# Performance work log

Measured on AMD Instinct MI355X. Metric: run time of the kernel, lower is better.

## Reference

```python
import jax, jax.numpy as jnp
import numpy as np

N_HEADS = 16


def setup_inputs() -> dict:
    key = jax.random.key(0)
    k1, k2, k3, k4, k5 = jax.random.split(key, 5)
    B, T, C = 2, 2048, 1024
    x = jax.random.normal(k1, (B, T, C), dtype=jnp.float32)
    rotary_cos_sin = jax.random.normal(k2, (T, C // N_HEADS), dtype=jnp.float32)  # unused by forward
    c = jax.random.normal(k3, (B, C), dtype=jnp.float32)  # unused by forward
    # Linear weights, torch convention: y = x @ W.T
    W_qkv = jax.random.normal(k4, (3 * C, C), dtype=jnp.float32) * (1.0 / np.sqrt(C))
    W_out = jax.random.normal(k5, (C, C), dtype=jnp.float32) * (1.0 / np.sqrt(C))
    return {"x": x, "rotary_cos_sin": rotary_cos_sin, "c": c, "W_qkv": W_qkv, "W_out": W_out}


def reference(x, rotary_cos_sin, c, W_qkv, W_out):
    B, T, C = x.shape
    H = N_HEADS
    D = C // H
    # qkv projection (no bias)
    qkv = jnp.einsum('btc,fc->btf', x, W_qkv)          # [B,T,3C]
    q, k, v = jnp.split(qkv, 3, axis=-1)
    q = q.reshape(B, T, H, D)
    k = k.reshape(B, T, H, D)
    v = v.reshape(B, T, H, D)
    # manual attention: full TxT score matrix, as in the original
    att = jnp.einsum('bthd,bshd->bhts', q, k) * (1.0 / jnp.sqrt(jnp.asarray(D, x.dtype)))
    att = jax.nn.softmax(att, axis=-1)
    # attn_dropout / resid_dropout are identity at inference
    y = jnp.einsum('bhts,bshd->bthd', att, v).reshape(B, T, C)
    return jnp.einsum('btc,oc->bto', y, W_out)
```

## Files before the change

### kernel.cpp

```cpp
#include <hip/hip_runtime.h>
#include <hip/hip_bf16.h>

typedef __bf16 bf16;
typedef __attribute__((ext_vector_type(8))) __bf16 bf16x8;
typedef __attribute__((ext_vector_type(4))) float f32x4;

#define MFMA16(A, B, C) __builtin_amdgcn_mfma_f32_16x16x32_bf16((A), (B), (C), 0, 0, 0)

__device__ __forceinline__ void gload_lds16(const void* g, void* l) {
    __builtin_amdgcn_global_load_lds(
        (const __attribute__((address_space(1))) void*)g,
        (__attribute__((address_space(3))) void*)l,
        16, 0, 0);
}

__global__ __launch_bounds__(256) void cast_f32_bf16(
    const float* __restrict__ in, bf16* __restrict__ out)
{
    const int i = (blockIdx.x * 256 + threadIdx.x) * 8;
    const float4 a = *(const float4*)(in + i);
    const float4 b = *(const float4*)(in + i + 4);
    bf16x8 o;
    o[0] = (bf16)a.x; o[1] = (bf16)a.y; o[2] = (bf16)a.z; o[3] = (bf16)a.w;
    o[4] = (bf16)b.x; o[5] = (bf16)b.y; o[6] = (bf16)b.z; o[7] = (bf16)b.w;
    *(bf16x8*)(out + i) = o;
}

template <typename OutT>
__global__ __launch_bounds__(256) void gemm_bt128(
    const bf16* __restrict__ A, const bf16* __restrict__ B, OutT* __restrict__ C,
    int M, int N, int K)
{
    constexpr int BK = 32;
    __shared__ __align__(16) bf16 sA[128 * BK];
    __shared__ __align__(16) bf16 sB[128 * BK];

    const int tid  = threadIdx.x;
    const int lane = tid & 63;
    const int wave = tid >> 6;
    const int wr   = wave >> 1;
    const int wc   = wave & 1;
    const int bm   = blockIdx.y * 128;
    const int bn   = blockIdx.x * 128;

    f32x4 acc[4][4] = {};

    const size_t ldb = (size_t)K * 2;
    const int srow = wave * 32 + (lane >> 2);
    const int scol = (lane & 3) * 16;
    const char* Ab = (const char*)A + (size_t)(bm + srow) * ldb + scol;
    const char* Bb = (const char*)B + (size_t)(bn + srow) * ldb + scol;
    char* ldsA = (char*)sA + wave * 2048;
    char* ldsB = (char*)sB + wave * 2048;

    const int arow = wr * 64 + (lane & 15);
    const int brow = wc * 64 + (lane & 15);
    const int koff = (lane >> 4) * 8;

    for (int k0 = 0; k0 < K; k0 += BK) {
        __syncthreads();
        const size_t kb = (size_t)k0 * 2;
        gload_lds16(Ab + kb,                ldsA);
        gload_lds16(Ab + kb + 16 * ldb,     ldsA + 1024);
        gload_lds16(Bb + kb,                ldsB);
        gload_lds16(Bb + kb + 16 * ldb,     ldsB + 1024);
        __syncthreads();

        bf16x8 af[4], bfr[4];
#pragma unroll
        for (int m = 0; m < 4; ++m)
            af[m] = *(const bf16x8*)&sA[(arow + m * 16) * BK + koff];
#pragma unroll
        for (int n = 0; n < 4; ++n)
            bfr[n] = *(const bf16x8*)&sB[(brow + n * 16) * BK + koff];
#pragma unroll
        for (int m = 0; m < 4; ++m)
#pragma unroll
            for (int n = 0; n < 4; ++n)
                acc[m][n] = MFMA16(af[m], bfr[n], acc[m][n]);
    }

    const int crow0 = bm + wr * 64 + (lane >> 4) * 4;
    const int ccol0 = bn + wc * 64 + (lane & 15);
#pragma unroll
    for (int m = 0; m < 4; ++m)
#pragma unroll
        for (int n = 0; n < 4; ++n)
#pragma unroll
            for (int j = 0; j < 4; ++j)
                C[(size_t)(crow0 + m * 16 + j) * N + ccol0 + n * 16] = (OutT)acc[m][n][j];
}

__global__ __launch_bounds__(256) void attn64(
    const bf16* __restrict__ qkv, bf16* __restrict__ y)
{
    constexpr int T = 2048, Cd = 1024, F = 3072, D = 64, KV = 64;
    __shared__ __align__(16) bf16 sK[KV * D];
    __shared__ __align__(16) bf16 sVT[D * 72];
    __shared__ __align__(16) bf16 sP[4 * 16 * 72];

    const int tid  = threadIdx.x;
    const int lane = tid & 63;
    const int wave = tid >> 6;
    const int bh = blockIdx.y;
    const int b  = bh >> 4, h = bh & 15;
    const int q0 = blockIdx.x * 64;

    const bf16* qkvb = qkv + (size_t)b * T * F;
    const int qcol = h * D;
    const int kcol = Cd + h * D;
    const int vcol = 2 * Cd + h * D;

    const int qrow = q0 + wave * 16 + (lane & 15);
    bf16x8 qf[2];
#pragma unroll
    for (int kk = 0; kk < 2; ++kk)
        qf[kk] = *(const bf16x8*)(qkvb + (size_t)qrow * F + qcol + kk * 32 + (lane >> 4) * 8);

    f32x4 oacc[4] = {};
    float m_r[4] = {-1e30f, -1e30f, -1e30f, -1e30f};
    float l_r[4] = {};

    const int ksrow  = wave * 16 + (lane >> 3);
    const int kdbyte = 16 * ((lane & 7) ^ (lane >> 3));
    bf16* sPw = sP + wave * 16 * 72;

    for (int s0 = 0; s0 < T; s0 += KV) {
        __syncthreads();
        gload_lds16((const char*)qkvb + ((size_t)(s0 + ksrow) * F + kcol) * 2 + kdbyte,
                    (char*)sK + wave * 2048);
        gload_lds16((const char*)qkvb + ((size_t)(s0 + ksrow + 8) * F + kcol) * 2 + kdbyte,
                    (char*)sK + wave * 2048 + 1024);
#pragma unroll
        for (int r = 0; r < 2; ++r) {
            const int d0 = wave * 8 + r * 32;
            bf16x8 v = *(const bf16x8*)(qkvb + (size_t)(s0 + lane) * F + vcol + d0);
#pragma unroll
            for (int i = 0; i < 8; ++i) sVT[(d0 + i) * 72 + lane] = v[i];
        }
        __syncthreads();

        f32x4 sacc[4] = {};
#pragma unroll
        for (int kk = 0; kk < 2; ++kk) {
#pragma unroll
            for (int j = 0; j < 4; ++j) {
                const int krow = (lane & 15) + 16 * j;
                const int dlog = kk * 64 + (lane >> 4) * 16;
                bf16x8 kf = *(const bf16x8*)((const char*)sK + krow * 128 + (dlog ^ ((krow & 7) << 4)));
                sacc[j] = MFMA16(qf[kk], kf, sacc[j]);
            }
        }

#pragma unroll
        for (int r = 0; r < 4; ++r) {
            float mx = fmaxf(fmaxf(sacc[0][r], sacc[1][r]), fmaxf(sacc[2][r], sacc[3][r])) * 0.125f;
#pragma unroll
            for (int m = 1; m < 16; m <<= 1) mx = fmaxf(mx, __shfl_xor(mx, m));
            const float mn = fmaxf(m_r[r], mx);
            const float al = __expf(m_r[r] - mn);
            m_r[r] = mn;
            float rs = 0.f;
#pragma unroll
            for (int j = 0; j < 4; ++j) {
                const float p = __expf(sacc[j][r] * 0.125f - mn);
                rs += p;
                sPw[((lane >> 4) * 4 + r) * 72 + (lane & 15) + 16 * j] = (bf16)p;
            }
            l_r[r] = l_r[r] * al + rs;
#pragma unroll
            for (int n = 0; n < 4; ++n) oacc[n][r] *= al;
        }

#pragma unroll
        for (int kk = 0; kk < 2; ++kk) {
            bf16x8 pa = *(const bf16x8*)&sPw[(lane & 15) * 72 + kk * 32 + (lane >> 4) * 8];
#pragma unroll
            for (int n = 0; n < 4; ++n) {
                bf16x8 vf = *(const bf16x8*)&sVT[((lane & 15) + 16 * n) * 72 + kk * 32 + (lane >> 4) * 8];
                oacc[n] = MFMA16(pa, vf, oacc[n]);
            }
        }
    }

#pragma unroll
    for (int r = 0; r < 4; ++r) {
        float ls = l_r[r];
#pragma unroll
        for (int m = 1; m < 16; m <<= 1) ls += __shfl_xor(ls, m);
        const float inv = 1.f / ls;
        const int t = q0 + wave * 16 + (lane >> 4) * 4 + r;
#pragma unroll
        for (int n = 0; n < 4; ++n)
            y[(size_t)(b * T + t) * Cd + h * D + (lane & 15) + 16 * n] = (bf16)(oacc[n][r] * inv);
    }
}

extern "C" void kernel_launch(void* const* d_in, const int* in_sizes, int n_in,
                              void* d_out, int out_size, void* d_ws, size_t ws_size,
                              hipStream_t stream) {
    (void)in_sizes; (void)n_in; (void)out_size; (void)ws_size;
    const float* x    = (const float*)d_in[0];
    const float* Wqkv = (const float*)d_in[3];
    const float* Wout = (const float*)d_in[4];
    float* out = (float*)d_out;

    bf16* xb    = (bf16*)d_ws;
    bf16* wqkvb = xb    + (size_t)4096 * 1024;
    bf16* woutb = wqkvb + (size_t)3072 * 1024;
    bf16* qkv   = woutb + (size_t)1024 * 1024;
    bf16* yb    = qkv   + (size_t)4096 * 3072;

    cast_f32_bf16<<<4096 * 1024 / 2048, 256, 0, stream>>>(x, xb);
    cast_f32_bf16<<<3072 * 1024 / 2048, 256, 0, stream>>>(Wqkv, wqkvb);
    cast_f32_bf16<<<1024 * 1024 / 2048, 256, 0, stream>>>(Wout, woutb);

    gemm_bt128<bf16><<<dim3(3072 / 128, 4096 / 128), 256, 0, stream>>>(xb, wqkvb, qkv, 4096, 3072, 1024);
    attn64<<<dim3(2048 / 64, 2 * 16), 256, 0, stream>>>(qkv, yb);
    gemm_bt128<float><<<dim3(1024 / 128, 4096 / 128), 256, 0, stream>>>(yb, woutb, out, 4096, 1024, 1024);
}
```

Measured before the change: 253.1 us.

## Rewrite attention with 32x32 MFMA, transposed LDS reads and register-resident P

Replaces the 16x16 MFMA flash-attention kernel with one using 32x32x16 MFMA, 128 queries per block and 32 per wave. S is computed as K·Q^T so the probabilities stay in registers and are repacked via lane shuffles rather than written to LDS. V is loaded asynchronously into LDS and read with ds_read_b64_tr_b16 transposing loads instead of a manual scalar transpose. Softmax switches to exp2 with a folded scale. It adds intricate index swizzling and manual waitcnt scheduling, which raises correctness risk.

```diff
diff --git a/kernel.cpp b/kernel.cpp
--- a/kernel.cpp
+++ b/kernel.cpp
@@ -2,16 +2,33 @@
 #include <hip/hip_bf16.h>
 
 typedef __bf16 bf16;
+typedef __attribute__((ext_vector_type(4))) __bf16 bf16x4;
 typedef __attribute__((ext_vector_type(8))) __bf16 bf16x8;
 typedef __attribute__((ext_vector_type(4))) float f32x4;
+typedef __attribute__((ext_vector_type(16))) float f32x16;
 
 #define MFMA16(A, B, C) __builtin_amdgcn_mfma_f32_16x16x32_bf16((A), (B), (C), 0, 0, 0)
+#define MFMA32(A, B, C) __builtin_amdgcn_mfma_f32_32x32x16_bf16((A), (B), (C), 0, 0, 0)
+
+union U8 { unsigned w[4]; bf16x8 v; };
 
 __device__ __forceinline__ void gload_lds16(const void* g, void* l) {
     __builtin_amdgcn_global_load_lds(
         (const __attribute__((address_space(1))) void*)g,
         (__attribute__((address_space(3))) void*)l,
         16, 0, 0);
+}
+
+__device__ __forceinline__ unsigned pk2(float a, float b) {
+    union { bf16 h[2]; unsigned u; } t;
+    t.h[0] = (bf16)a; t.h[1] = (bf16)b;
+    return t.u;
+}
+
+__device__ __forceinline__ unsigned long long tr16(unsigned addr) {
+    unsigned long long r;
+    asm volatile("ds_read_b64_tr_b16 %0, %1" : "=v"(r) : "v"(addr));
+    return r;
 }
 
 __global__ __launch_bounds__(256) void cast_f32_bf16(
@@ -60,10 +77,10 @@
     for (int k0 = 0; k0 < K; k0 += BK) {
         __syncthreads();
         const size_t kb = (size_t)k0 * 2;
-        gload_lds16(Ab + kb,                ldsA);
-        gload_lds16(Ab + kb + 16 * ldb,     ldsA + 1024);
-        gload_lds16(Bb + kb,                ldsB);
-        gload_lds16(Bb + kb + 16 * ldb,     ldsB + 1024);
+        gload_lds16(Ab + kb,            ldsA);
+        gload_lds16(Ab + kb + 16 * ldb, ldsA + 1024);
+        gload_lds16(Bb + kb,            ldsB);
+        gload_lds16(Bb + kb + 16 * ldb, ldsB + 1024);
         __syncthreads();
 
         bf16x8 af[4], bfr[4];
@@ -91,109 +108,173 @@
                 C[(size_t)(crow0 + m * 16 + j) * N + ccol0 + n * 16] = (OutT)acc[m][n][j];
 }
 
-__global__ __launch_bounds__(256) void attn64(
+__global__ __launch_bounds__(256, 2) void attn32(
     const bf16* __restrict__ qkv, bf16* __restrict__ y)
 {
-    constexpr int T = 2048, Cd = 1024, F = 3072, D = 64, KV = 64;
-    __shared__ __align__(16) bf16 sK[KV * D];
-    __shared__ __align__(16) bf16 sVT[D * 72];
-    __shared__ __align__(16) bf16 sP[4 * 16 * 72];
-
-    const int tid  = threadIdx.x;
-    const int lane = tid & 63;
-    const int wave = tid >> 6;
-    const int bh = blockIdx.y;
-    const int b  = bh >> 4, h = bh & 15;
-    const int q0 = blockIdx.x * 64;
-
+    constexpr int T = 2048, F = 3072, Cd = 1024;
+    constexpr float c1 = 0.18033688011112042f;
+
+    __shared__ __align__(16) bf16 sK[64 * 64];
+    __shared__ __align__(16) bf16 sV[64 * 64];
+
+    const int tid = threadIdx.x, lane = tid & 63, wave = tid >> 6;
+    const int hi = lane >> 5, q5 = lane & 31;
+    const int bh = blockIdx.y, b = bh >> 4, h = bh & 15;
     const bf16* qkvb = qkv + (size_t)b * T * F;
-    const int qcol = h * D;
-    const int kcol = Cd + h * D;
-    const int vcol = 2 * Cd + h * D;
-
-    const int qrow = q0 + wave * 16 + (lane & 15);
-    bf16x8 qf[2];
-#pragma unroll
-    for (int kk = 0; kk < 2; ++kk)
-        qf[kk] = *(const bf16x8*)(qkvb + (size_t)qrow * F + qcol + kk * 32 + (lane >> 4) * 8);
-
-    f32x4 oacc[4] = {};
-    float m_r[4] = {-1e30f, -1e30f, -1e30f, -1e30f};
-    float l_r[4] = {};
-
-    const int ksrow  = wave * 16 + (lane >> 3);
-    const int kdbyte = 16 * ((lane & 7) ^ (lane >> 3));
-    bf16* sPw = sP + wave * 16 * 72;
-
-    for (int s0 = 0; s0 < T; s0 += KV) {
+    const int qcol = h * 64, kcol = Cd + h * 64, vcol = 2 * Cd + h * 64;
+
+    const int gq = blockIdx.x * 128 + wave * 32 + q5;
+    bf16x8 qf[4];
+#pragma unroll
+    for (int s = 0; s < 4; ++s)
+        qf[s] = *(const bf16x8*)(qkvb + (size_t)gq * F + qcol + s * 16 + hi * 8);
+
+    const int ck0 = (wave * 2 + 0) * 64 + lane, ck1 = ck0 + 64;
+    const int kvk0 = ck0 >> 3, d0k0 = ((ck0 & 7) ^ (kvk0 & 7)) << 3;
+    const int kvk1 = ck1 >> 3, d0k1 = ((ck1 & 7) ^ (kvk1 & 7)) << 3;
+    const int cv0 = ck0, cv1 = ck1;
+    const int kvv0 = ((cv0 >> 1) & 3) | (((cv0 >> 5) & 1) << 2) | (((cv0 >> 4) & 1) << 3) | (((cv0 >> 6) & 3) << 4);
+    const int dv0  = ((cv0 & 1) << 3) | (((cv0 >> 3) & 1) << 4) | (((cv0 >> 8) & 1) << 5);
+    const int kvv1 = ((cv1 >> 1) & 3) | (((cv1 >> 5) & 1) << 2) | (((cv1 >> 4) & 1) << 3) | (((cv1 >> 6) & 3) << 4);
+    const int dv1  = ((cv1 & 1) << 3) | (((cv1 >> 3) & 1) << 4) | (((cv1 >> 8) & 1) << 5);
+
+    const char* kq0 = (const char*)qkvb + (size_t)(kvk0 * F + kcol + d0k0) * 2;
+    const char* kq1 = (const char*)qkvb + (size_t)(kvk1 * F + kcol + d0k1) * 2;
+    const char* vq0 = (const char*)qkvb + (size_t)(kvv0 * F + vcol + dv0) * 2;
+    const char* vq1 = (const char*)qkvb + (size_t)(kvv1 * F + vcol + dv1) * 2;
+    char* dstK0 = (char*)sK + (wave * 2 + 0) * 1024;
+    char* dstK1 = (char*)sK + (wave * 2 + 1) * 1024;
+    char* dstV0 = (char*)sV + (wave * 2 + 0) * 1024;
+    char* dstV1 = (char*)sV + (wave * 2 + 1) * 1024;
+
+    const unsigned sVoff = (unsigned)(uintptr_t)(__attribute__((address_space(3))) char*)(void*)sV;
+    const unsigned trb = sVoff + 8u * (unsigned)lane;
+
+    const unsigned swz = (unsigned)(q5 & 7) << 4;
+
+    f32x16 oacc[2] = {};
+    float m_run = -3e38f, l_run = 0.f;
+
+    for (int s0 = 0; s0 < T; s0 += 64) {
         __syncthreads();
-        gload_lds16((const char*)qkvb + ((size_t)(s0 + ksrow) * F + kcol) * 2 + kdbyte,
-                    (char*)sK + wave * 2048);
-        gload_lds16((const char*)qkvb + ((size_t)(s0 + ksrow + 8) * F + kcol) * 2 + kdbyte,
-                    (char*)sK + wave * 2048 + 1024);
-#pragma unroll
-        for (int r = 0; r < 2; ++r) {
-            const int d0 = wave * 8 + r * 32;
-            bf16x8 v = *(const bf16x8*)(qkvb + (size_t)(s0 + lane) * F + vcol + d0);
-#pragma unroll
-            for (int i = 0; i < 8; ++i) sVT[(d0 + i) * 72 + lane] = v[i];
-        }
+        const size_t sb = (size_t)s0 * F * 2;
+        gload_lds16(kq0 + sb, dstK0);
+        gload_lds16(kq1 + sb, dstK1);
+        gload_lds16(vq0 + sb, dstV0);
+        gload_lds16(vq1 + sb, dstV1);
         __syncthreads();
 
-        f32x4 sacc[4] = {};
-#pragma unroll
-        for (int kk = 0; kk < 2; ++kk) {
-#pragma unroll
-            for (int j = 0; j < 4; ++j) {
-                const int krow = (lane & 15) + 16 * j;
-                const int dlog = kk * 64 + (lane >> 4) * 16;
-                bf16x8 kf = *(const bf16x8*)((const char*)sK + krow * 128 + (dlog ^ ((krow & 7) << 4)));
-                sacc[j] = MFMA16(qf[kk], kf, sacc[j]);
+        f32x16 sacc[2];
+#pragma unroll
+        for (int a = 0; a < 2; ++a) {
+            f32x16 acc = {};
+#pragma unroll
+            for (int dsl = 0; dsl < 4; ++dsl) {
+                const unsigned cbyte = ((unsigned)(dsl * 32 + hi * 16)) ^ swz;
+                bf16x8 kf = *(const bf16x8*)((const char*)sK + (a * 32 + q5) * 128 + cbyte);
+                acc = MFMA32(kf, qf[dsl], acc);
             }
-        }
-
-#pragma unroll
-        for (int r = 0; r < 4; ++r) {
-            float mx = fmaxf(fmaxf(sacc[0][r], sacc[1][r]), fmaxf(sacc[2][r], sacc[3][r])) * 0.125f;
-#pragma unroll
-            for (int m = 1; m < 16; m <<= 1) mx = fmaxf(mx, __shfl_xor(mx, m));
-            const float mn = fmaxf(m_r[r], mx);
-            const float al = __expf(m_r[r] - mn);
-            m_r[r] = mn;
-            float rs = 0.f;
-#pragma unroll
-            for (int j = 0; j < 4; ++j) {
-                const float p = __expf(sacc[j][r] * 0.125f - mn);
-                rs += p;
-                sPw[((lane >> 4) * 4 + r) * 72 + (lane & 15) + 16 * j] = (bf16)p;
+            sacc[a] = acc;
+        }
+
+        float mt = -3e38f;
+#pragma unroll
+        for (int a = 0; a < 2; ++a)
+#pragma unroll
+            for (int r = 0; r < 16; ++r) mt = fmaxf(mt, sacc[a][r]);
+        mt = fmaxf(mt, __shfl_xor(mt, 32));
+        const float mn = fmaxf(m_run, mt);
+        const float al = __builtin_exp2f((m_run - mn) * c1);
+        m_run = mn;
+        const float mc = mn * c1;
+
+        float rs = 0.f;
+        unsigned W[2][4][2];
+#pragma unroll
+        for (int a = 0; a < 2; ++a)
+#pragma unroll
+            for (int bb = 0; bb < 4; ++bb) {
+                const float p0 = __builtin_exp2f(fmaf(sacc[a][4 * bb + 0], c1, -mc));
+                const float p1 = __builtin_exp2f(fmaf(sacc[a][4 * bb + 1], c1, -mc));
+                const float p2 = __builtin_exp2f(fmaf(sacc[a][4 * bb + 2], c1, -mc));
+                const float p3 = __builtin_exp2f(fmaf(sacc[a][4 * bb + 3], c1, -mc));
+                rs += (p0 + p1) + (p2 + p3);
+                W[a][bb][0] = pk2(p0, p1);
+                W[a][bb][1] = pk2(p2, p3);
             }
-            l_r[r] = l_r[r] * al + rs;
-#pragma unroll
-            for (int n = 0; n < 4; ++n) oacc[n][r] *= al;
-        }
-
-#pragma unroll
-        for (int kk = 0; kk < 2; ++kk) {
-            bf16x8 pa = *(const bf16x8*)&sPw[(lane & 15) * 72 + kk * 32 + (lane >> 4) * 8];
-#pragma unroll
-            for (int n = 0; n < 4; ++n) {
-                bf16x8 vf = *(const bf16x8*)&sVT[((lane & 15) + 16 * n) * 72 + kk * 32 + (lane >> 4) * 8];
-                oacc[n] = MFMA16(pa, vf, oacc[n]);
+        l_run = fmaf(l_run, al, rs);
+#pragma unroll
+        for (int d = 0; d < 2; ++d)
+#pragma unroll
+            for (int r = 0; r < 16; ++r) oacc[d][r] *= al;
+
+        unsigned Zz[2][2][2];
+#pragma unroll
+        for (int a = 0; a < 2; ++a)
+#pragma unroll
+            for (int c = 0; c < 2; ++c)
+#pragma unroll
+                for (int w = 0; w < 2; ++w) {
+                    const unsigned yv = hi ? W[a][2 * c][w] : W[a][2 * c + 1][w];
+                    Zz[a][c][w] = (unsigned)__shfl_xor((int)yv, 32);
+                }
+        bf16x8 pb[4];
+#pragma unroll
+        for (int a = 0; a < 2; ++a)
+#pragma unroll
+            for (int c = 0; c < 2; ++c) {
+                U8 u;
+                u.w[0] = hi ? Zz[a][c][0] : W[a][2 * c][0];
+                u.w[1] = hi ? Zz[a][c][1] : W[a][2 * c][1];
+                u.w[2] = hi ? W[a][2 * c + 1][0] : Zz[a][c][0];
+                u.w[3] = hi ? W[a][2 * c + 1][1] : Zz[a][c][1];
+                pb[2 * a + c] = u.v;
             }
+
+        unsigned long long t0[8], t1[8];
+#pragma unroll
+        for (int ks = 0; ks < 4; ++ks) {
+            t0[2 * ks + 0] = tr16(trb + (unsigned)(ks * 1024));
+            t0[2 * ks + 1] = tr16(trb + (unsigned)(ks * 1024 + 512));
+        }
+#pragma unroll
+        for (int ks = 0; ks < 4; ++ks) {
+            t1[2 * ks + 0] = tr16(trb + (unsigned)(4096 + ks * 1024));
+            t1[2 * ks + 1] = tr16(trb + (unsigned)(4096 + ks * 1024 + 512));
+        }
+        asm volatile("s_waitcnt lgkmcnt(8)" ::: "memory");
+        __builtin_amdgcn_sched_barrier(0);
+#pragma unroll
+        for (int ks = 0; ks < 4; ++ks) {
+            U8 u;
+            u.w[0] = (unsigned)t0[2 * ks];     u.w[1] = (unsigned)(t0[2 * ks] >> 32);
+            u.w[2] = (unsigned)t0[2 * ks + 1]; u.w[3] = (unsigned)(t0[2 * ks + 1] >> 32);
+            oacc[0] = MFMA32(u.v, pb[ks], oacc[0]);
+        }
+        asm volatile("s_waitcnt lgkmcnt(0)" ::: "memory");
+        __builtin_amdgcn_sched_barrier(0);
+#pragma unroll
+        for (int ks = 0; ks < 4; ++ks) {
+            U8 u;
+            u.w[0] = (unsigned)t1[2 * ks];     u.w[1] = (unsigned)(t1[2 * ks] >> 32);
+            u.w[2] = (unsigned)t1[2 * ks + 1]; u.w[3] = (unsigned)(t1[2 * ks + 1] >> 32);
+            oacc[1] = MFMA32(u.v, pb[ks], oacc[1]);
         }
     }
 
-#pragma unroll
-    for (int r = 0; r < 4; ++r) {
-        float ls = l_r[r];
-#pragma unroll
-        for (int m = 1; m < 16; m <<= 1) ls += __shfl_xor(ls, m);
-        const float inv = 1.f / ls;
-        const int t = q0 + wave * 16 + (lane >> 4) * 4 + r;
-#pragma unroll
-        for (int n = 0; n < 4; ++n)
-            y[(size_t)(b * T + t) * Cd + h * D + (lane & 15) + 16 * n] = (bf16)(oacc[n][r] * inv);
-    }
+    const float lt = l_run + __shfl_xor(l_run, 32);
+    const float inv = 1.f / lt;
+    bf16* yrow = y + (size_t)(b * T + gq) * Cd + h * 64;
+#pragma unroll
+    for (int d = 0; d < 2; ++d)
+#pragma unroll
+        for (int bb = 0; bb < 4; ++bb) {
+            bf16x4 o4;
+#pragma unroll
+            for (int jj = 0; jj < 4; ++jj)
+                o4[jj] = (bf16)(oacc[d][4 * bb + jj] * inv);
+            *(bf16x4*)(yrow + d * 32 + 8 * bb + 4 * hi) = o4;
+        }
 }
 
 extern "C" void kernel_launch(void* const* d_in, const int* in_sizes, int n_in,
@@ -216,6 +297,6 @@
     cast_f32_bf16<<<1024 * 1024 / 2048, 256, 0, stream>>>(Wout, woutb);
 
     gemm_bt128<bf16><<<dim3(3072 / 128, 4096 / 128), 256, 0, stream>>>(xb, wqkvb, qkv, 4096, 3072, 1024);
-    attn64<<<dim3(2048 / 64, 2 * 16), 256, 0, stream>>>(qkv, yb);
+    attn32<<<dim3(2048 / 128, 2 * 16), 256, 0, stream>>>(qkv, yb);
     gemm_bt128<float><<<dim3(1024 / 128, 4096 / 128), 256, 0, stream>>>(yb, woutb, out, 4096, 1024, 1024);
 }
```

After: 229.9 us. 1.1x faster.
